# Kernel optimization log

Measured on AMD Instinct MI355X. Metric: run time of the kernel, lower is better.

Reference implementation:

```python
import jax, jax.numpy as jnp
import numpy as np

N, E, DIM, H = 50000, 800000, 64, 2
HD = H * DIM


def setup_inputs() -> dict:
    key = jax.random.key(0)
    ks = jax.random.split(key, 16)
    s = 0.05
    return {
        "x": jax.random.normal(ks[0], (N, DIM), jnp.float32),
        "edge_index": jax.random.randint(ks[1], (2, E), 0, N, jnp.int64),
        "Wq": jax.random.normal(ks[2], (DIM, HD), jnp.float32) * s,
        "bq": jax.random.normal(ks[3], (HD,), jnp.float32) * s,
        "Wk": jax.random.normal(ks[4], (DIM, HD), jnp.float32) * s,
        "bk": jax.random.normal(ks[5], (HD,), jnp.float32) * s,
        "Wv": jax.random.normal(ks[6], (DIM, HD), jnp.float32) * s,
        "bv": jax.random.normal(ks[7], (HD,), jnp.float32) * s,
        "Wskip": jax.random.normal(ks[8], (DIM, HD), jnp.float32) * s,
        "bskip": jax.random.normal(ks[9], (HD,), jnp.float32) * s,
        "Wc": jax.random.normal(ks[10], (HD, DIM), jnp.float32) * s,
        "bc": jax.random.normal(ks[11], (DIM,), jnp.float32) * s,
        "gamma": jnp.ones((DIM,), jnp.float32),
        "beta": jnp.zeros((DIM,), jnp.float32),
    }


def reference(x, edge_index, Wq, bq, Wk, bk, Wv, bv, Wskip, bskip, Wc, bc, gamma, beta):
    src, dst = edge_index[0], edge_index[1]  # messages flow src -> dst
    # TransformerConv: per-head q/k/v projections, [N, H, D]
    q = (x @ Wq + bq).reshape(N, H, DIM)
    k = (x @ Wk + bk).reshape(N, H, DIM)
    v = (x @ Wv + bv).reshape(N, H, DIM)
    scale = 1.0 / np.sqrt(DIM).astype(np.float32)
    # edge-wise attention logits: [E, H]
    alpha = jnp.einsum('ehd,ehd->eh', q[dst], k[src]) * scale
    # segment softmax over incoming edges of each dst node (PyG softmax)
    amax = jax.ops.segment_max(alpha, dst, num_segments=N)
    a = jnp.exp(alpha - amax[dst])
    asum = jax.ops.segment_sum(a, dst, num_segments=N)
    a = a / (asum[dst] + 1e-16)
    # weighted scatter-aggregate of values: [N, H, D] -> concat heads
    out = jax.ops.segment_sum(a[:, :, None] * v[src], dst, num_segments=N)
    out = out.reshape(N, HD)
    # root/skip connection (root_weight=True default)
    out = out + (x @ Wskip + bskip)
    # concat linear: H*D -> dim
    out = out @ Wc + bc
    # pyg.LayerNorm default mode='graph': normalize over ALL nodes+features
    out = out - out.mean()
    out = out / (out.std() + 1e-5)  # std with unbiased=False (jnp default ddof=0)
    return out * gamma + beta
```

## Files before the change

kernel.cpp:

```cpp
#include <hip/hip_runtime.h>
#include <hip/hip_bf16.h>

#define N_NODES 50000
#define N_EDGES 800000
#define DIM 64
#define NHEAD 2
#define HD 128
#define NCOL 448
#define MAXDEG 64

#define NBIN 196
#define BCAP 6144
#define ACH 2048
#define BIN_BLKS 391

#define PREP_B 112
#define PROJ_B 782

typedef short bf16x8 __attribute__((ext_vector_type(8)));
typedef float f32x16 __attribute__((ext_vector_type(16)));
typedef float f32x2 __attribute__((ext_vector_type(2)));

__device__ __forceinline__ unsigned short f2bf(float f) {
    unsigned u = __float_as_uint(f);
    unsigned r = (u + 0x7fffu + ((u >> 16) & 1u)) >> 16;
    return (unsigned short)r;
}
__device__ __forceinline__ unsigned char f2fp8(float f) {
    int r = __builtin_amdgcn_cvt_pk_fp8_f32(f, f, 0, false);
    return (unsigned char)(r & 0xff);
}

__global__ __launch_bounds__(256) void k_pb(
    const int* __restrict__ ei,
    const float* __restrict__ Wq, const float* __restrict__ bq,
    const float* __restrict__ Wk, const float* __restrict__ bk,
    const float* __restrict__ Wv, const float* __restrict__ bv,
    const float* __restrict__ Wskip, const float* __restrict__ bskip,
    const float* __restrict__ Wc, const float* __restrict__ bc,
    unsigned short* __restrict__ WallT, float* __restrict__ ball,
    int* __restrict__ bincnt, unsigned* __restrict__ bins,
    double* __restrict__ stats)
{
    const int t = threadIdx.x;
    if (blockIdx.x < PREP_B) {
        int gid = blockIdx.x * 256 + t;
        if (gid == 0) { stats[0] = 0.0; stats[1] = 0.0; }
        const int j = gid >> 6;
        const int d = gid & 63;
        float w, bb;
        if (j < 128) {
            w = Wq[d * HD + j] * 0.125f;
            bb = bq[j] * 0.125f;
        } else if (j < 256) {
            int jj = j - 128;
            w = Wk[d * HD + jj];
            bb = bk[jj];
        } else if (j < 384) {
            int jj = j - 256;
            int h = jj >> 6, jc = jj & 63;
            float s = 0.f, sb = 0.f;
            for (int c = 0; c < 64; c++) {
                float wc = Wc[(h * 64 + c) * DIM + jc];
                s  += Wv[d * HD + h * 64 + c] * wc;
                sb += bv[h * 64 + c] * wc;
            }
            w = s; bb = sb;
        } else {
            int jj = j - 384;
            float s = 0.f, sb = bc[jj];
            for (int c = 0; c < HD; c++) {
                float wc = Wc[c * DIM + jj];
                s  += Wskip[d * HD + c] * wc;
                sb += bskip[c] * wc;
            }
            w = s; bb = sb;
        }
        WallT[gid] = f2bf(w);
        if (d == 0) ball[j] = bb;
        return;
    }
    __shared__ unsigned pk[ACH];
    __shared__ unsigned char bbn[ACH];
    __shared__ unsigned ord[ACH];
    __shared__ int hist[256];
    __shared__ int lofs[256];
    __shared__ int gbase[256];
    const int e0 = (blockIdx.x - PREP_B) * ACH;
    hist[t] = 0;
    __syncthreads();
    for (int i = t; i < ACH; i += 256) {
        int e = e0 + i;
        if (e < N_EDGES) {
            int src = ei[e];
            int d = ei[N_EDGES + e];
            int bin = d >> 8;
            pk[i] = (unsigned)(((d & 255) << 16) | src);
            bbn[i] = (unsigned char)bin;
            atomicAdd(&hist[bin], 1);
        } else {
            bbn[i] = 255;
        }
    }
    __syncthreads();
    int h = hist[t];
    lofs[t] = h;
    __syncthreads();
    for (int off = 1; off < 256; off <<= 1) {
        int add = (t >= off) ? lofs[t - off] : 0;
        __syncthreads();
        lofs[t] += add;
        __syncthreads();
    }
    int excl = lofs[t] - h;
    if (t < NBIN && h > 0) gbase[t] = atomicAdd(&bincnt[t], h);
    __syncthreads();
    lofs[t] = excl;
    hist[t] = 0;
    __syncthreads();
    for (int i = t; i < ACH; i += 256) {
        int bin = bbn[i];
        if (bin != 255) {
            int sl = atomicAdd(&hist[bin], 1);
            ord[lofs[bin] + sl] = pk[i];
        }
    }
    __syncthreads();
    const int w = t >> 6, lane = t & 63;
    for (int bin = w; bin < NBIN; bin += 4) {
        int cnt = hist[bin];
        int lo = lofs[bin];
        int gb = gbase[bin];
        for (int i = lane; i < cnt; i += 64) {
            int pos = gb + i;
            if (pos < BCAP) bins[(size_t)bin * BCAP + pos] = ord[lo + i];
        }
    }
}

__global__ __launch_bounds__(256) void k_ep(
    const float* __restrict__ x,
    const unsigned short* __restrict__ WallT, const float* __restrict__ ball,
    float* __restrict__ q, unsigned char* __restrict__ kv, float* __restrict__ skipc,
    const int* __restrict__ bincnt, const unsigned* __restrict__ bins,
    int* __restrict__ deg, int* __restrict__ elist)
{
    const int blk = blockIdx.x;
    const int t = threadIdx.x;
    if (blk >= PROJ_B) {
        const int bin = blk - PROJ_B;
        __shared__ int nodecnt[256];
        nodecnt[t] = 0;
        __syncthreads();
        int cnt = bincnt[bin]; if (cnt > BCAP) cnt = BCAP;
        const unsigned* bp = bins + (size_t)bin * BCAP;
        for (int i = t; i < cnt; i += 256) {
            unsigned p = bp[i];
            int local = p >> 16;
            int src = p & 0xffff;
            int sl = atomicAdd(&nodecnt[local], 1);
            if (sl < MAXDEG)
                elist[((size_t)((bin << 8) | local)) * MAXDEG + sl] = src;
        }
        __syncthreads();
        int node = (bin << 8) + t;
        if (node < N_NODES) {
            int dgv = nodecnt[t];
            deg[node] = dgv > MAXDEG ? MAXDEG : dgv;
        }
        return;
    }
    const int w = t >> 6;
    const int lane = t & 63;
    const int col = lane & 31;
    const int khalf = lane >> 5;
    const int n0 = blk * 64 + (w >> 1) * 32;
    const int ct0 = (w & 1) * 7;
    const int rowbase = 4 * khalf;

    int nread = n0 + col; if (nread >= N_NODES) nread = N_NODES - 1;
    const float* ap = x + (size_t)nread * 64 + khalf * 8;
    bf16x8 afrag[4];
#pragma unroll
    for (int kk = 0; kk < 4; kk++) {
        float4 xa = *((const float4*)(ap + kk * 16));
        float4 xb4 = *((const float4*)(ap + kk * 16 + 4));
        bf16x8 f;
        f[0] = (short)f2bf(xa.x); f[1] = (short)f2bf(xa.y);
        f[2] = (short)f2bf(xa.z); f[3] = (short)f2bf(xa.w);
        f[4] = (short)f2bf(xb4.x); f[5] = (short)f2bf(xb4.y);
        f[6] = (short)f2bf(xb4.z); f[7] = (short)f2bf(xb4.w);
        afrag[kk] = f;
    }

    for (int tt = 0; tt < 7; tt++) {
        const int gc = (ct0 + tt) * 32 + col;
        const float b = ball[gc];
        f32x16 acc;
#pragma unroll
        for (int r = 0; r < 16; r++) acc[r] = b;
        const unsigned short* bp = WallT + (size_t)gc * 64 + khalf * 8;
#pragma unroll
        for (int kk = 0; kk < 4; kk++) {
            bf16x8 bfrag = *((const bf16x8*)(bp + kk * 16));
            acc = __builtin_amdgcn_mfma_f32_32x32x16_bf16(afrag[kk], bfrag, acc, 0, 0, 0);
        }
        if (gc < 128) {
#pragma unroll
            for (int r = 0; r < 16; r++) {
                int node = n0 + (r & 3) + 8 * (r >> 2) + rowbase;
                if (node < N_NODES) q[(size_t)node * HD + gc] = acc[r];
            }
        } else if (gc < 384) {
            int ch = gc - 128;
#pragma unroll
            for (int r = 0; r < 16; r++) {
                int node = n0 + (r & 3) + 8 * (r >> 2) + rowbase;
                if (node < N_NODES) kv[(size_t)node * 256 + ch] = f2fp8(acc[r]);
            }
        } else {
#pragma unroll
            for (int r = 0; r < 16; r++) {
                int node = n0 + (r & 3) + 8 * (r >> 2) + rowbase;
                if (node < N_NODES) skipc[(size_t)node * DIM + (gc - 384)] = acc[r];
            }
        }
    }
}

__global__ __launch_bounds__(256) void k_attn(
    const float* __restrict__ q, const unsigned char* __restrict__ kv,
    const float* __restrict__ skipc,
    const int* __restrict__ deg, const int* __restrict__ elist,
    float* __restrict__ out, float* __restrict__ parts)
{
    const int w = threadIdx.x >> 6;
    const int lane = threadIdx.x & 63;
    const int g = lane >> 3;
    const int j = lane & 7;
    const int n = blockIdx.x * 4 + w;
    const float4* qp = (const float4*)(q + (size_t)n * HD);
    const float4 qa = qp[2 * j],      qb = qp[2 * j + 1];
    const float4 qc = qp[16 + 2 * j], qd = qp[17 + 2 * j];
    const int myE = elist[(size_t)n * MAXDEG + lane];
    float acc0[8], acc1[8];
#pragma unroll
    for (int i = 0; i < 8; i++) { acc0[i] = 0.f; acc1[i] = 0.f; }
    float l0 = 0.f, l1 = 0.f;
    int dg = deg[n]; if (dg > MAXDEG) dg = MAXDEG;
    for (int b0 = 0; b0 < dg; b0 += 8) {
        int idx = b0 + g;
        bool valid = idx < dg;
        int s = __shfl(myE, valid ? idx : 0, 64);
        const uint2* kp = (const uint2*)(kv + (size_t)s * 256);
        uint2 K0 = kp[j], K1 = kp[8 + j];
        uint2 V0 = kp[16 + j], V1 = kp[24 + j];
        f32x2 k0a = __builtin_amdgcn_cvt_pk_f32_fp8(K0.x, false);
        f32x2 k0b = __builtin_amdgcn_cvt_pk_f32_fp8(K0.x, true);
        f32x2 k0c = __builtin_amdgcn_cvt_pk_f32_fp8(K0.y, false);
        f32x2 k0d = __builtin_amdgcn_cvt_pk_f32_fp8(K0.y, true);
        f32x2 k1a = __builtin_amdgcn_cvt_pk_f32_fp8(K1.x, false);
        f32x2 k1b = __builtin_amdgcn_cvt_pk_f32_fp8(K1.x, true);
        f32x2 k1c = __builtin_amdgcn_cvt_pk_f32_fp8(K1.y, false);
        f32x2 k1d = __builtin_amdgcn_cvt_pk_f32_fp8(K1.y, true);
        float p0 = qa.x * k0a[0] + qa.y * k0a[1] + qa.z * k0b[0] + qa.w * k0b[1]
                 + qb.x * k0c[0] + qb.y * k0c[1] + qb.z * k0d[0] + qb.w * k0d[1];
        float p1 = qc.x * k1a[0] + qc.y * k1a[1] + qc.z * k1b[0] + qc.w * k1b[1]
                 + qd.x * k1c[0] + qd.y * k1c[1] + qd.z * k1d[0] + qd.w * k1d[1];
#pragma unroll
        for (int off = 1; off < 8; off <<= 1) {
            p0 += __shfl_xor(p0, off, 64);
            p1 += __shfl_xor(p1, off, 64);
        }
        float w0 = valid ? __expf(p0) : 0.f;
        float w1 = valid ? __expf(p1) : 0.f;
        l0 += w0; l1 += w1;
        f32x2 v0a = __builtin_amdgcn_cvt_pk_f32_fp8(V0.x, false);
        f32x2 v0b = __builtin_amdgcn_cvt_pk_f32_fp8(V0.x, true);
        f32x2 v0c = __builtin_amdgcn_cvt_pk_f32_fp8(V0.y, false);
        f32x2 v0d = __builtin_amdgcn_cvt_pk_f32_fp8(V0.y, true);
        f32x2 v1a = __builtin_amdgcn_cvt_pk_f32_fp8(V1.x, false);
        f32x2 v1b = __builtin_amdgcn_cvt_pk_f32_fp8(V1.x, true);
        f32x2 v1c = __builtin_amdgcn_cvt_pk_f32_fp8(V1.y, false);
        f32x2 v1d = __builtin_amdgcn_cvt_pk_f32_fp8(V1.y, true);
        acc0[0] += w0 * v0a[0]; acc0[1] += w0 * v0a[1];
        acc0[2] += w0 * v0b[0]; acc0[3] += w0 * v0b[1];
        acc0[4] += w0 * v0c[0]; acc0[5] += w0 * v0c[1];
        acc0[6] += w0 * v0d[0]; acc0[7] += w0 * v0d[1];
        acc1[0] += w1 * v1a[0]; acc1[1] += w1 * v1a[1];
        acc1[2] += w1 * v1b[0]; acc1[3] += w1 * v1b[1];
        acc1[4] += w1 * v1c[0]; acc1[5] += w1 * v1c[1];
        acc1[6] += w1 * v1d[0]; acc1[7] += w1 * v1d[1];
    }
#pragma unroll
    for (int off = 8; off < 64; off <<= 1) {
        l0 += __shfl_xor(l0, off, 64);
        l1 += __shfl_xor(l1, off, 64);
#pragma unroll
        for (int i = 0; i < 8; i++) {
            acc0[i] += __shfl_xor(acc0[i], off, 64);
            acc1[i] += __shfl_xor(acc1[i], off, 64);
        }
    }
    if (g == 0) {
        float inv0 = 1.f / (l0 + 1e-16f), inv1 = 1.f / (l1 + 1e-16f);
        const float4* sk = (const float4*)(skipc + (size_t)n * DIM);
        float4 sa = sk[2 * j], sb = sk[2 * j + 1];
        float o[8];
        o[0] = acc0[0] * inv0 + acc1[0] * inv1 + sa.x;
        o[1] = acc0[1] * inv0 + acc1[1] * inv1 + sa.y;
        o[2] = acc0[2] * inv0 + acc1[2] * inv1 + sa.z;
        o[3] = acc0[3] * inv0 + acc1[3] * inv1 + sa.w;
        o[4] = acc0[4] * inv0 + acc1[4] * inv1 + sb.x;
        o[5] = acc0[5] * inv0 + acc1[5] * inv1 + sb.y;
        o[6] = acc0[6] * inv0 + acc1[6] * inv1 + sb.z;
        o[7] = acc0[7] * inv0 + acc1[7] * inv1 + sb.w;
        float4 r0 = {o[0], o[1], o[2], o[3]}, r1 = {o[4], o[5], o[6], o[7]};
        float4* op = (float4*)(out + (size_t)n * DIM);
        op[2 * j] = r0; op[2 * j + 1] = r1;
        float s_ = 0.f, ss = 0.f;
#pragma unroll
        for (int i = 0; i < 8; i++) { s_ += o[i]; ss += o[i] * o[i]; }
#pragma unroll
        for (int off = 1; off < 8; off <<= 1) {
            s_ += __shfl_xor(s_, off, 64);
            ss += __shfl_xor(ss, off, 64);
        }
        if (j == 0) { parts[n * 2 + 0] = s_; parts[n * 2 + 1] = ss; }
    }
}

#define RED_BLOCKS 100
__global__ __launch_bounds__(256) void k_reduce(
    const float* __restrict__ parts, double* __restrict__ stats)
{
    double s = 0.0, ss = 0.0;
    for (int i = blockIdx.x * 256 + threadIdx.x; i < N_NODES; i += RED_BLOCKS * 256) {
        s  += (double)parts[i * 2 + 0];
        ss += (double)parts[i * 2 + 1];
    }
#pragma unroll
    for (int off = 32; off > 0; off >>= 1) {
        s  += __shfl_down(s, off);
        ss += __shfl_down(ss, off);
    }
    __shared__ double sdd[8];
    int wave = threadIdx.x >> 6;
    if ((threadIdx.x & 63) == 0) { sdd[wave * 2] = s; sdd[wave * 2 + 1] = ss; }
    __syncthreads();
    if (threadIdx.x == 0) {
        double S = 0.0, SS = 0.0;
        for (int w = 0; w < 4; w++) { S += sdd[w * 2]; SS += sdd[w * 2 + 1]; }
        atomicAdd(&stats[0], S);
        atomicAdd(&stats[1], SS);
    }
}

__global__ __launch_bounds__(256) void k_norm(
    float* __restrict__ out, const double* __restrict__ stats,
    const float* __restrict__ gamma, const float* __restrict__ beta)
{
    int i = blockIdx.x * 256 + threadIdx.x;
    if (i >= N_NODES * DIM / 4) return;
    const double cnt = (double)N_NODES * (double)DIM;
    double mean = stats[0] / cnt;
    double var  = stats[1] / cnt - mean * mean;
    if (var < 0.0) var = 0.0;
    float mf = (float)mean;
    float inv = 1.0f / ((float)sqrt(var) + 1e-5f);
    float4 v = ((const float4*)out)[i];
    float4 gv = ((const float4*)gamma)[i & 15];
    float4 bv2 = ((const float4*)beta)[i & 15];
    v.x = (v.x - mf) * inv * gv.x + bv2.x;
    v.y = (v.y - mf) * inv * gv.y + bv2.y;
    v.z = (v.z - mf) * inv * gv.z + bv2.z;
    v.w = (v.w - mf) * inv * gv.w + bv2.w;
    ((float4*)out)[i] = v;
}

extern "C" void kernel_launch(void* const* d_in, const int* in_sizes, int n_in,
                              void* d_out, int out_size, void* d_ws, size_t ws_size,
                              hipStream_t stream) {
    const float* x     = (const float*)d_in[0];
    const int*   ei    = (const int*)d_in[1];
    const float* Wq    = (const float*)d_in[2];
    const float* bq    = (const float*)d_in[3];
    const float* Wk    = (const float*)d_in[4];
    const float* bk    = (const float*)d_in[5];
    const float* Wv    = (const float*)d_in[6];
    const float* bv    = (const float*)d_in[7];
    const float* Wsk   = (const float*)d_in[8];
    const float* bsk   = (const float*)d_in[9];
    const float* Wc    = (const float*)d_in[10];
    const float* bc    = (const float*)d_in[11];
    const float* gamma = (const float*)d_in[12];
    const float* beta  = (const float*)d_in[13];
    float* out = (float*)d_out;

    float* ws = (float*)d_ws;
    const size_t NF = (size_t)N_NODES * HD;
    float* q = ws;
    unsigned char* kv = (unsigned char*)(ws + NF);
    float* skipc = (float*)(kv + (size_t)N_NODES * 256);
    unsigned short* WallT = (unsigned short*)(skipc + (size_t)N_NODES * DIM);
    float* ball   = (float*)(WallT + NCOL * 64);
    int* bincnt   = (int*)(ball + NCOL);
    unsigned* bins = (unsigned*)(bincnt + 256);
    int* deg      = (int*)(bins + (size_t)NBIN * BCAP);
    int* elist    = deg + N_NODES;
    float* parts  = (float*)(elist + (size_t)N_NODES * MAXDEG);
    double* stats = (double*)(parts + (size_t)N_NODES * 2);

    hipMemsetAsync(bincnt, 0, NBIN * sizeof(int), stream);
    hipLaunchKernelGGL(k_pb, dim3(PREP_B + BIN_BLKS), dim3(256), 0, stream,
                       ei, Wq, bq, Wk, bk, Wv, bv, Wsk, bsk, Wc, bc,
                       WallT, ball, bincnt, bins, stats);
    hipLaunchKernelGGL(k_ep, dim3(PROJ_B + NBIN), dim3(256), 0, stream,
                       x, WallT, ball, q, kv, skipc, bincnt, bins, deg, elist);
    hipLaunchKernelGGL(k_attn, dim3(N_NODES / 4), dim3(256), 0, stream,
                       q, kv, skipc, deg, elist, out, parts);
    hipLaunchKernelGGL(k_reduce, dim3(RED_BLOCKS), dim3(256), 0, stream, parts, stats);
    hipLaunchKernelGGL(k_norm, dim3(N_NODES * DIM / 4 / 256 + 1), dim3(256), 0, stream,
                       out, stats, gamma, beta);
}
```

Measured before the change: 188.6 us.

## Narrow edge list to 16-bit, unroll attention by two edges, use exp2 scaling

Source indices in the per-node edge list are stored as 16-bit values instead of 32-bit, which halves that buffer's footprint and read traffic. The attention loop now handles 16 edges per iteration with two independent gather streams to expose more memory-level parallelism. It uses packed f32x2 multiply-adds, and it folds log2(e) into the Q scale so the hardware exp2 can be used. The partial-sum layout is changed to structure-of-arrays for coalesced reduction reads. The 16-bit indices rely on the source index already fitting in 16 bits from the bin packing, and the unrolling raises register pressure.

```diff
diff --git a/kernel.cpp b/kernel.cpp
--- a/kernel.cpp
+++ b/kernel.cpp
@@ -16,6 +16,8 @@
 
 #define PREP_B 112
 #define PROJ_B 782
+
+#define QSCALE 0.18033688011112042f
 
 typedef short bf16x8 __attribute__((ext_vector_type(8)));
 typedef float f32x16 __attribute__((ext_vector_type(16)));
@@ -50,8 +52,8 @@
         const int d = gid & 63;
         float w, bb;
         if (j < 128) {
-            w = Wq[d * HD + j] * 0.125f;
-            bb = bq[j] * 0.125f;
+            w = Wq[d * HD + j] * QSCALE;
+            bb = bq[j] * QSCALE;
         } else if (j < 256) {
             int jj = j - 128;
             w = Wk[d * HD + jj];
@@ -143,7 +145,7 @@
     const unsigned short* __restrict__ WallT, const float* __restrict__ ball,
     float* __restrict__ q, unsigned char* __restrict__ kv, float* __restrict__ skipc,
     const int* __restrict__ bincnt, const unsigned* __restrict__ bins,
-    int* __restrict__ deg, int* __restrict__ elist)
+    int* __restrict__ deg, unsigned short* __restrict__ elist)
 {
     const int blk = blockIdx.x;
     const int t = threadIdx.x;
@@ -160,7 +162,7 @@
             int src = p & 0xffff;
             int sl = atomicAdd(&nodecnt[local], 1);
             if (sl < MAXDEG)
-                elist[((size_t)((bin << 8) | local)) * MAXDEG + sl] = src;
+                elist[((size_t)((bin << 8) | local)) * MAXDEG + sl] = (unsigned short)src;
         }
         __syncthreads();
         int node = (bin << 8) + t;
@@ -231,7 +233,7 @@
 __global__ __launch_bounds__(256) void k_attn(
     const float* __restrict__ q, const unsigned char* __restrict__ kv,
     const float* __restrict__ skipc,
-    const int* __restrict__ deg, const int* __restrict__ elist,
+    const int* __restrict__ deg, const unsigned short* __restrict__ elist,
     float* __restrict__ out, float* __restrict__ parts)
 {
     const int w = threadIdx.x >> 6;
@@ -239,67 +241,91 @@
     const int g = lane >> 3;
     const int j = lane & 7;
     const int n = blockIdx.x * 4 + w;
-    const float4* qp = (const float4*)(q + (size_t)n * HD);
-    const float4 qa = qp[2 * j],      qb = qp[2 * j + 1];
-    const float4 qc = qp[16 + 2 * j], qd = qp[17 + 2 * j];
+    const f32x2* qp = (const f32x2*)(q + (size_t)n * HD);
+    f32x2 q0[4], q1[4];
+#pragma unroll
+    for (int i = 0; i < 4; i++) { q0[i] = qp[4 * j + i]; q1[i] = qp[32 + 4 * j + i]; }
     const int myE = elist[(size_t)n * MAXDEG + lane];
-    float acc0[8], acc1[8];
-#pragma unroll
-    for (int i = 0; i < 8; i++) { acc0[i] = 0.f; acc1[i] = 0.f; }
+    f32x2 acc0[4], acc1[4];
+#pragma unroll
+    for (int i = 0; i < 4; i++) {
+        acc0[i] = (f32x2){0.f, 0.f};
+        acc1[i] = (f32x2){0.f, 0.f};
+    }
     float l0 = 0.f, l1 = 0.f;
     int dg = deg[n]; if (dg > MAXDEG) dg = MAXDEG;
-    for (int b0 = 0; b0 < dg; b0 += 8) {
-        int idx = b0 + g;
-        bool valid = idx < dg;
-        int s = __shfl(myE, valid ? idx : 0, 64);
-        const uint2* kp = (const uint2*)(kv + (size_t)s * 256);
-        uint2 K0 = kp[j], K1 = kp[8 + j];
-        uint2 V0 = kp[16 + j], V1 = kp[24 + j];
-        f32x2 k0a = __builtin_amdgcn_cvt_pk_f32_fp8(K0.x, false);
-        f32x2 k0b = __builtin_amdgcn_cvt_pk_f32_fp8(K0.x, true);
-        f32x2 k0c = __builtin_amdgcn_cvt_pk_f32_fp8(K0.y, false);
-        f32x2 k0d = __builtin_amdgcn_cvt_pk_f32_fp8(K0.y, true);
-        f32x2 k1a = __builtin_amdgcn_cvt_pk_f32_fp8(K1.x, false);
-        f32x2 k1b = __builtin_amdgcn_cvt_pk_f32_fp8(K1.x, true);
-        f32x2 k1c = __builtin_amdgcn_cvt_pk_f32_fp8(K1.y, false);
-        f32x2 k1d = __builtin_amdgcn_cvt_pk_f32_fp8(K1.y, true);
-        float p0 = qa.x * k0a[0] + qa.y * k0a[1] + qa.z * k0b[0] + qa.w * k0b[1]
-                 + qb.x * k0c[0] + qb.y * k0c[1] + qb.z * k0d[0] + qb.w * k0d[1];
-        float p1 = qc.x * k1a[0] + qc.y * k1a[1] + qc.z * k1b[0] + qc.w * k1b[1]
-                 + qd.x * k1c[0] + qd.y * k1c[1] + qd.z * k1d[0] + qd.w * k1d[1];
+    for (int b0 = 0; b0 < dg; b0 += 16) {
+        int iA = b0 + g, iB = b0 + 8 + g;
+        bool vA = iA < dg, vB = iB < dg;
+        int sA = __shfl(myE, vA ? iA : 0, 64);
+        int sB = __shfl(myE, vB ? iB : 0, 64);
+        const uint2* kpA = (const uint2*)(kv + (size_t)sA * 256);
+        const uint2* kpB = (const uint2*)(kv + (size_t)sB * 256);
+        uint2 KA0 = kpA[j],      KA1 = kpA[8 + j];
+        uint2 VA0 = kpA[16 + j], VA1 = kpA[24 + j];
+        uint2 KB0 = kpB[j],      KB1 = kpB[8 + j];
+        uint2 VB0 = kpB[16 + j], VB1 = kpB[24 + j];
+        f32x2 pa0 = q0[0] * __builtin_amdgcn_cvt_pk_f32_fp8(KA0.x, false);
+        pa0 += q0[1] * __builtin_amdgcn_cvt_pk_f32_fp8(KA0.x, true);
+        pa0 += q0[2] * __builtin_amdgcn_cvt_pk_f32_fp8(KA0.y, false);
+        pa0 += q0[3] * __builtin_amdgcn_cvt_pk_f32_fp8(KA0.y, true);
+        f32x2 pa1 = q1[0] * __builtin_amdgcn_cvt_pk_f32_fp8(KA1.x, false);
+        pa1 += q1[1] * __builtin_amdgcn_cvt_pk_f32_fp8(KA1.x, true);
+        pa1 += q1[2] * __builtin_amdgcn_cvt_pk_f32_fp8(KA1.y, false);
+        pa1 += q1[3] * __builtin_amdgcn_cvt_pk_f32_fp8(KA1.y, true);
+        float p0A = pa0[0] + pa0[1];
+        float p1A = pa1[0] + pa1[1];
+        f32x2 pb0 = q0[0] * __builtin_amdgcn_cvt_pk_f32_fp8(KB0.x, false);
+        pb0 += q0[1] * __builtin_amdgcn_cvt_pk_f32_fp8(KB0.x, true);
+        pb0 += q0[2] * __builtin_amdgcn_cvt_pk_f32_fp8(KB0.y, false);
+        pb0 += q0[3] * __builtin_amdgcn_cvt_pk_f32_fp8(KB0.y, true);
+        f32x2 pb1 = q1[0] * __builtin_amdgcn_cvt_pk_f32_fp8(KB1.x, false);
+        pb1 += q1[1] * __builtin_amdgcn_cvt_pk_f32_fp8(KB1.x, true);
+        pb1 += q1[2] * __builtin_amdgcn_cvt_pk_f32_fp8(KB1.y, false);
+        pb1 += q1[3] * __builtin_amdgcn_cvt_pk_f32_fp8(KB1.y, true);
+        float p0B = pb0[0] + pb0[1];
+        float p1B = pb1[0] + pb1[1];
 #pragma unroll
         for (int off = 1; off < 8; off <<= 1) {
-            p0 += __shfl_xor(p0, off, 64);
-            p1 += __shfl_xor(p1, off, 64);
-        }
-        float w0 = valid ? __expf(p0) : 0.f;
-        float w1 = valid ? __expf(p1) : 0.f;
-        l0 += w0; l1 += w1;
-        f32x2 v0a = __builtin_amdgcn_cvt_pk_f32_fp8(V0.x, false);
-        f32x2 v0b = __builtin_amdgcn_cvt_pk_f32_fp8(V0.x, true);
-        f32x2 v0c = __builtin_amdgcn_cvt_pk_f32_fp8(V0.y, false);
-        f32x2 v0d = __builtin_amdgcn_cvt_pk_f32_fp8(V0.y, true);
-        f32x2 v1a = __builtin_amdgcn_cvt_pk_f32_fp8(V1.x, false);
-        f32x2 v1b = __builtin_amdgcn_cvt_pk_f32_fp8(V1.x, true);
-        f32x2 v1c = __builtin_amdgcn_cvt_pk_f32_fp8(V1.y, false);
-        f32x2 v1d = __builtin_amdgcn_cvt_pk_f32_fp8(V1.y, true);
-        acc0[0] += w0 * v0a[0]; acc0[1] += w0 * v0a[1];
-        acc0[2] += w0 * v0b[0]; acc0[3] += w0 * v0b[1];
-        acc0[4] += w0 * v0c[0]; acc0[5] += w0 * v0c[1];
-        acc0[6] += w0 * v0d[0]; acc0[7] += w0 * v0d[1];
-        acc1[0] += w1 * v1a[0]; acc1[1] += w1 * v1a[1];
-        acc1[2] += w1 * v1b[0]; acc1[3] += w1 * v1b[1];
-        acc1[4] += w1 * v1c[0]; acc1[5] += w1 * v1c[1];
-        acc1[6] += w1 * v1d[0]; acc1[7] += w1 * v1d[1];
-    }
+            p0A += __shfl_xor(p0A, off, 64);
+            p1A += __shfl_xor(p1A, off, 64);
+            p0B += __shfl_xor(p0B, off, 64);
+            p1B += __shfl_xor(p1B, off, 64);
+        }
+        float w0A = vA ? __builtin_amdgcn_exp2f(p0A) : 0.f;
+        float w1A = vA ? __builtin_amdgcn_exp2f(p1A) : 0.f;
+        float w0B = vB ? __builtin_amdgcn_exp2f(p0B) : 0.f;
+        float w1B = vB ? __builtin_amdgcn_exp2f(p1B) : 0.f;
+        l0 += w0A + w0B; l1 += w1A + w1B;
+        f32x2 w0Av = {w0A, w0A}, w1Av = {w1A, w1A};
+        f32x2 w0Bv = {w0B, w0B}, w1Bv = {w1B, w1B};
+        acc0[0] += w0Av * __builtin_amdgcn_cvt_pk_f32_fp8(VA0.x, false);
+        acc0[1] += w0Av * __builtin_amdgcn_cvt_pk_f32_fp8(VA0.x, true);
+        acc0[2] += w0Av * __builtin_amdgcn_cvt_pk_f32_fp8(VA0.y, false);
+        acc0[3] += w0Av * __builtin_amdgcn_cvt_pk_f32_fp8(VA0.y, true);
+        acc1[0] += w1Av * __builtin_amdgcn_cvt_pk_f32_fp8(VA1.x, false);
+        acc1[1] += w1Av * __builtin_amdgcn_cvt_pk_f32_fp8(VA1.x, true);
+        acc1[2] += w1Av * __builtin_amdgcn_cvt_pk_f32_fp8(VA1.y, false);
+        acc1[3] += w1Av * __builtin_amdgcn_cvt_pk_f32_fp8(VA1.y, true);
+        acc0[0] += w0Bv * __builtin_amdgcn_cvt_pk_f32_fp8(VB0.x, false);
+        acc0[1] += w0Bv * __builtin_amdgcn_cvt_pk_f32_fp8(VB0.x, true);
+        acc0[2] += w0Bv * __builtin_amdgcn_cvt_pk_f32_fp8(VB0.y, false);
+        acc0[3] += w0Bv * __builtin_amdgcn_cvt_pk_f32_fp8(VB0.y, true);
+        acc1[0] += w1Bv * __builtin_amdgcn_cvt_pk_f32_fp8(VB1.x, false);
+        acc1[1] += w1Bv * __builtin_amdgcn_cvt_pk_f32_fp8(VB1.x, true);
+        acc1[2] += w1Bv * __builtin_amdgcn_cvt_pk_f32_fp8(VB1.y, false);
+        acc1[3] += w1Bv * __builtin_amdgcn_cvt_pk_f32_fp8(VB1.y, true);
+    }
+    float* a0 = (float*)acc0;
+    float* a1 = (float*)acc1;
 #pragma unroll
     for (int off = 8; off < 64; off <<= 1) {
         l0 += __shfl_xor(l0, off, 64);
         l1 += __shfl_xor(l1, off, 64);
 #pragma unroll
         for (int i = 0; i < 8; i++) {
-            acc0[i] += __shfl_xor(acc0[i], off, 64);
-            acc1[i] += __shfl_xor(acc1[i], off, 64);
+            a0[i] += __shfl_xor(a0[i], off, 64);
+            a1[i] += __shfl_xor(a1[i], off, 64);
         }
     }
     if (g == 0) {
@@ -307,14 +333,14 @@
         const float4* sk = (const float4*)(skipc + (size_t)n * DIM);
         float4 sa = sk[2 * j], sb = sk[2 * j + 1];
         float o[8];
-        o[0] = acc0[0] * inv0 + acc1[0] * inv1 + sa.x;
-        o[1] = acc0[1] * inv0 + acc1[1] * inv1 + sa.y;
-        o[2] = acc0[2] * inv0 + acc1[2] * inv1 + sa.z;
-        o[3] = acc0[3] * inv0 + acc1[3] * inv1 + sa.w;
-        o[4] = acc0[4] * inv0 + acc1[4] * inv1 + sb.x;
-        o[5] = acc0[5] * inv0 + acc1[5] * inv1 + sb.y;
-        o[6] = acc0[6] * inv0 + acc1[6] * inv1 + sb.z;
-        o[7] = acc0[7] * inv0 + acc1[7] * inv1 + sb.w;
+        o[0] = a0[0] * inv0 + a1[0] * inv1 + sa.x;
+        o[1] = a0[1] * inv0 + a1[1] * inv1 + sa.y;
+        o[2] = a0[2] * inv0 + a1[2] * inv1 + sa.z;
+        o[3] = a0[3] * inv0 + a1[3] * inv1 + sa.w;
+        o[4] = a0[4] * inv0 + a1[4] * inv1 + sb.x;
+        o[5] = a0[5] * inv0 + a1[5] * inv1 + sb.y;
+        o[6] = a0[6] * inv0 + a1[6] * inv1 + sb.z;
+        o[7] = a0[7] * inv0 + a1[7] * inv1 + sb.w;
         float4 r0 = {o[0], o[1], o[2], o[3]}, r1 = {o[4], o[5], o[6], o[7]};
         float4* op = (float4*)(out + (size_t)n * DIM);
         op[2 * j] = r0; op[2 * j + 1] = r1;
@@ -326,7 +352,7 @@
             s_ += __shfl_xor(s_, off, 64);
             ss += __shfl_xor(ss, off, 64);
         }
-        if (j == 0) { parts[n * 2 + 0] = s_; parts[n * 2 + 1] = ss; }
+        if (j == 0) { parts[n] = s_; parts[N_NODES + n] = ss; }
     }
 }
 
@@ -336,8 +362,8 @@
 {
     double s = 0.0, ss = 0.0;
     for (int i = blockIdx.x * 256 + threadIdx.x; i < N_NODES; i += RED_BLOCKS * 256) {
-        s  += (double)parts[i * 2 + 0];
-        ss += (double)parts[i * 2 + 1];
+        s  += (double)parts[i];
+        ss += (double)parts[N_NODES + i];
     }
 #pragma unroll
     for (int off = 32; off > 0; off >>= 1) {
@@ -407,8 +433,8 @@
     int* bincnt   = (int*)(ball + NCOL);
     unsigned* bins = (unsigned*)(bincnt + 256);
     int* deg      = (int*)(bins + (size_t)NBIN * BCAP);
-    int* elist    = deg + N_NODES;
-    float* parts  = (float*)(elist + (size_t)N_NODES * MAXDEG);
+    unsigned short* elist = (unsigned short*)(deg + N_NODES);
+    float* parts  = (float*)(elist + (size_t)NBIN * 256 * MAXDEG);
     double* stats = (double*)(parts + (size_t)N_NODES * 2);
 
     hipMemsetAsync(bincnt, 0, NBIN * sizeof(int), stream);
```

Result: no change. 190.1 us (+0.8%).
